# Performance work log

Hardware: AMD Instinct MI355X
Metric: run time of the kernel (lower is better)

The kernel has to match this reference:

```python
import jax, jax.numpy as jnp
import numpy as np

N_NODES = 10000
N_EDGES = 320000
D_NODE = 128
D_EDGE = 32
D_IN = 2 * D_NODE + D_EDGE  # 288, concat(sender, receiver, edge)
D_HID = 192                 # AutoMLP log-spaced hidden dim between 288 and 128
D_OUT = 128


def setup_inputs() -> dict:
    key = jax.random.key(0)
    ks = jax.random.split(key, 8)
    n_embed = jax.random.normal(ks[0], (N_NODES, D_NODE), dtype=jnp.float32)
    e_embed = jax.random.normal(ks[1], (N_EDGES, D_EDGE), dtype=jnp.float32)
    senders = jnp.sort(jax.random.randint(ks[2], (N_EDGES,), 0, N_NODES, dtype=jnp.int32))
    receivers = jax.random.randint(ks[3], (N_EDGES,), 0, N_NODES, dtype=jnp.int32)
    # AutoMLP parameters (lecun_normal-style scaling)
    W1 = jax.random.normal(ks[4], (D_IN, D_HID), dtype=jnp.float32) / np.sqrt(D_IN)
    b1 = jnp.zeros((D_HID,), dtype=jnp.float32)
    W2 = jax.random.normal(ks[5], (D_HID, D_OUT), dtype=jnp.float32) / np.sqrt(D_HID)
    b2 = jnp.zeros((D_OUT,), dtype=jnp.float32)
    return {"n_embed": n_embed, "e_embed": e_embed, "senders": senders,
            "receivers": receivers, "W1": W1, "b1": b1, "W2": W2, "b2": b2}


def reference(n_embed, e_embed, senders, receivers, W1, b1, W2, b2):
    # gather sender/receiver node embeddings and concat with edge features: [E, 288]
    inp = jnp.concatenate([n_embed[senders], n_embed[receivers], e_embed], axis=-1)
    # AutoMLP: Dense -> tanh -> Dense (final layer linear)
    h = jnp.tanh(inp @ W1 + b1)          # [E, 192]
    msg = h @ W2 + b2                    # [E, 128]
    # segment_mean over senders (sorted), num_segments = n_nodes
    seg_sum = jax.ops.segment_sum(msg, senders, num_segments=N_NODES,
                                  indices_are_sorted=True)
    counts = jax.ops.segment_sum(jnp.ones((msg.shape[0],), dtype=msg.dtype), senders,
                                 num_segments=N_NODES, indices_are_sorted=True)
    return seg_sum / jnp.maximum(counts, 1.0)[:, None]
```

## Files before the change

### kernel.cpp

```cpp
#include <hip/hip_runtime.h>

#define E_TOT 320000
#define NN    10000
#define DN    128
#define DE    32
#define DH    192
#define DO    128
#define EB    64
#define SHS   196

typedef __attribute__((ext_vector_type(8))) short bf16x8;
typedef __attribute__((ext_vector_type(4))) float f32x4;

#define W1_FRAGS (8*12*64)
#define E_FRAGS  (12*64)
#define W2_FRAGS (6*8*64)
#define FRAGS_TOT (W1_FRAGS + E_FRAGS + W2_FRAGS)
__device__ __align__(16) unsigned short g_p1[W1_FRAGS * 8];
__device__ __align__(16) unsigned short g_e [E_FRAGS * 8];
__device__ __align__(16) unsigned short g_p2[W2_FRAGS * 8];

__device__ __forceinline__ unsigned short f2bf(float f) {
    union { float f; unsigned u; } v; v.f = f;
    return (unsigned short)((v.u + 0x7FFFu + ((v.u >> 16) & 1u)) >> 16);
}
__device__ __forceinline__ float bflo(unsigned u) {
    union { unsigned v; float f; } t; t.v = u << 16; return t.f;
}
__device__ __forceinline__ float bfhi(unsigned u) {
    union { unsigned v; float f; } t; t.v = u & 0xFFFF0000u; return t.f;
}
__device__ __forceinline__ float bf2f(unsigned short s) {
    union { unsigned v; float f; } t; t.v = (unsigned)s << 16; return t.f;
}
__device__ __forceinline__ float tanh_fast(float x) {
    float ex = __expf(x + x);
    return 1.0f - 2.0f * __builtin_amdgcn_rcpf(ex + 1.0f);
}
__device__ __forceinline__ unsigned cvt_pk_bf16(float lo, float hi) {
    unsigned r;
    asm("v_cvt_pk_bf16_f32 %0, %1, %2" : "=v"(r) : "v"(lo), "v"(hi));
    return r;
}

__global__ void prep(const float* __restrict__ W1, const float* __restrict__ W2)
{
    int f = blockIdx.x * 256 + threadIdx.x;
    unsigned short tmp[8];
    if (f < W1_FRAGS) {
        int kk = f / (12 * 64), nt = (f >> 6) % 12, lane = f & 63;
        int r0 = kk * 32 + ((lane >> 4) << 3);
        int c  = nt * 16 + (lane & 15);
        #pragma unroll
        for (int i = 0; i < 8; ++i) tmp[i] = f2bf(W1[(r0 + i) * DH + c]);
        *(uint4*)(g_p1 + (size_t)f * 8) = *(const uint4*)tmp;
    } else if (f < W1_FRAGS + E_FRAGS) {
        int f2 = f - W1_FRAGS;
        int mt = f2 >> 6, lane = f2 & 63;
        int k0 = ((lane >> 4) << 3);
        int hid = mt * 16 + (lane & 15);
        #pragma unroll
        for (int i = 0; i < 8; ++i) tmp[i] = f2bf(W1[(256 + k0 + i) * DH + hid]);
        *(uint4*)(g_e + (size_t)f2 * 8) = *(const uint4*)tmp;
    } else if (f < FRAGS_TOT) {
        int f3 = f - W1_FRAGS - E_FRAGS;
        int kk = f3 / (8 * 64), nt = (f3 >> 6) % 8, lane = f3 & 63;
        int r0 = kk * 32 + ((lane >> 4) << 3);
        int c  = nt * 16 + (lane & 15);
        #pragma unroll
        for (int i = 0; i < 8; ++i) tmp[i] = f2bf(W2[(r0 + i) * DO + c]);
        *(uint4*)(g_p2 + (size_t)f3 * 8) = *(const uint4*)tmp;
    }
}

__global__ __launch_bounds__(256) void node_proj(
    const float* __restrict__ n_embed, const float* __restrict__ b1,
    unsigned short* __restrict__ P)
{
    __shared__ __align__(16) unsigned short s_a[64][136];
    const int tid  = threadIdx.x;
    const int half = blockIdx.y;
    const int n0   = blockIdx.x * 64;

    #pragma unroll
    for (int it = 0; it < 8; ++it) {
        int idx = tid + it * 256;
        int row = idx >> 5, c = idx & 31;
        float4 v = make_float4(0.f, 0.f, 0.f, 0.f);
        if (n0 + row < NN) v = ((const float4*)(n_embed + (size_t)(n0 + row) * DN))[c];
        unsigned t0 = cvt_pk_bf16(v.x, v.y), t1 = cvt_pk_bf16(v.z, v.w);
        *(uint2*)&s_a[row][c * 4] = make_uint2(t0, t1);
    }
    __syncthreads();

    const int lane = tid & 63, w = tid >> 6;
    const int arow = lane & 15, akb = (lane >> 4) * 8, rbase = (lane >> 4) * 4;

    f32x4 acc[4][3];
    #pragma unroll
    for (int mt = 0; mt < 4; ++mt)
        #pragma unroll
        for (int j = 0; j < 3; ++j) acc[mt][j] = (f32x4){0.f, 0.f, 0.f, 0.f};

    for (int kk = 0; kk < 4; ++kk) {
        bf16x8 a[4], b[3];
        #pragma unroll
        for (int mt = 0; mt < 4; ++mt)
            a[mt] = *(const bf16x8*)&s_a[mt * 16 + arow][kk * 32 + akb];
        #pragma unroll
        for (int j = 0; j < 3; ++j)
            b[j] = *(const bf16x8*)(g_p1 + (((size_t)(kk + 4 * half) * 12 + (3 * w + j)) * 64 + lane) * 8);
        #pragma unroll
        for (int mt = 0; mt < 4; ++mt)
            #pragma unroll
            for (int j = 0; j < 3; ++j)
                acc[mt][j] = __builtin_amdgcn_mfma_f32_16x16x32_bf16(a[mt], b[j], acc[mt][j], 0, 0, 0);
    }

    unsigned short* Pout = P + (size_t)half * NN * DH;
    float bj[3];
    #pragma unroll
    for (int j = 0; j < 3; ++j) bj[j] = (half == 0) ? b1[48 * w + 16 * j + arow] : 0.f;
    const int gq = arow >> 2, ii = arow & 3;
    #pragma unroll
    for (int mt = 0; mt < 4; ++mt)
        #pragma unroll
        for (int j = 0; j < 3; ++j)
            #pragma unroll
            for (int r = 0; r < 4; ++r) {
                int row = n0 + mt * 16 + rbase + r;
                if (row < NN)
                    Pout[((size_t)row * 4 + gq) * 48 + (3 * w + j) * 4 + ii] =
                        f2bf(acc[mt][j][r] + bj[j]);
            }
}

__global__ __launch_bounds__(256) void edge_reduce(
    const float* __restrict__ e_embed,
    const int* __restrict__ senders, const int* __restrict__ receivers,
    const unsigned short* __restrict__ Ps, const unsigned short* __restrict__ Pr,
    float* __restrict__ Hbar)
{
    __shared__ __align__(16) unsigned short s_h[EB][SHS];
    __shared__ int s_send[EB];

    const int tid  = threadIdx.x;
    const int nb8  = gridDim.x >> 3;
    const int e0   = (((blockIdx.x & 7) * nb8) + (blockIdx.x >> 3)) * EB;
    const int lane = tid & 63, w = tid >> 6;
    const int arow = lane & 15, g = lane >> 4;

    const int myedge = e0 + w * 16 + arow;
    const int sN = senders[myedge], rN = receivers[myedge];
    const unsigned short* psbase = Ps + ((size_t)sN * 4 + g) * 48;
    const unsigned short* prbase = Pr + ((size_t)rN * 4 + g) * 48;
    uint4 psq[6], prq[6];
    #pragma unroll
    for (int j = 0; j < 6; ++j) {
        psq[j] = *(const uint4*)(psbase + j * 8);
        prq[j] = *(const uint4*)(prbase + j * 8);
    }
    union { bf16x8 v; unsigned u[4]; } bfr;
    {
        const float* erow = e_embed + (size_t)myedge * DE + g * 8;
        float4 ev0 = *(const float4*)erow;
        float4 ev1 = *(const float4*)(erow + 4);
        bfr.u[0] = cvt_pk_bf16(ev0.x, ev0.y);
        bfr.u[1] = cvt_pk_bf16(ev0.z, ev0.w);
        bfr.u[2] = cvt_pk_bf16(ev1.x, ev1.y);
        bfr.u[3] = cvt_pk_bf16(ev1.z, ev1.w);
    }
    if (tid < EB) s_send[tid] = senders[e0 + tid];

    #pragma unroll
    for (int mt = 0; mt < 12; ++mt) {
        unsigned px, py, qx, qy;
        if ((mt & 1) == 0) {
            px = psq[mt >> 1].x; py = psq[mt >> 1].y;
            qx = prq[mt >> 1].x; qy = prq[mt >> 1].y;
        } else {
            px = psq[mt >> 1].z; py = psq[mt >> 1].w;
            qx = prq[mt >> 1].z; qy = prq[mt >> 1].w;
        }
        bf16x8 af = *(const bf16x8*)(g_e + ((size_t)mt * 64 + lane) * 8);
        f32x4 z = (f32x4){0.f, 0.f, 0.f, 0.f};
        f32x4 acc = __builtin_amdgcn_mfma_f32_16x16x32_bf16(af, bfr.v, z, 0, 0, 0);
        float t0 = tanh_fast(acc[0] + bflo(px) + bflo(qx));
        float t1 = tanh_fast(acc[1] + bfhi(px) + bfhi(qx));
        float t2 = tanh_fast(acc[2] + bflo(py) + bflo(qy));
        float t3 = tanh_fast(acc[3] + bfhi(py) + bfhi(qy));
        *(uint2*)&s_h[w * 16 + arow][mt * 16 + g * 4] =
            make_uint2(cvt_pk_bf16(t0, t1), cvt_pk_bf16(t2, t3));
    }
    __syncthreads();

    if (tid < DH) {
        const int c = tid;
        float sum = 0.f;
        int cur = s_send[0];
        #pragma unroll 8
        for (int e = 0; e < EB; ++e) {
            sum += bf2f(s_h[e][c]);
            int nxt = (e + 1 < EB) ? s_send[e + 1] : -1;
            if (nxt != cur) {
                atomicAdd(&Hbar[(size_t)cur * DH + c], sum);
                sum = 0.f;
                cur = nxt;
            }
        }
    }
}

__global__ __launch_bounds__(256) void node_out(
    const float* __restrict__ Hbar, const int* __restrict__ senders,
    const float* __restrict__ b2, float* __restrict__ out)
{
    const int tid  = threadIdx.x;
    const int lane = tid & 63, w = tid >> 6;
    const int n0   = (blockIdx.x * 4 + w) * 16;
    if (n0 >= NN) return;
    const int arow = lane & 15, akb = (lane >> 4) * 8, rbase = (lane >> 4) * 4;

    const int myrow = (n0 + arow < NN) ? (n0 + arow) : (NN - 1);
    float ic;
    {
        int lo = 0, hi = E_TOT;
        while (lo < hi) { int m = (lo + hi) >> 1; if (senders[m] < myrow) lo = m + 1; else hi = m; }
        int s0 = lo;
        hi = E_TOT;
        while (lo < hi) { int m = (lo + hi) >> 1; if (senders[m] < myrow + 1) lo = m + 1; else hi = m; }
        int cnt = lo - s0;
        ic = (cnt > 0) ? 1.0f / (float)cnt : 0.0f;
    }

    const float* hrow = Hbar + (size_t)myrow * DH;
    union { bf16x8 v; unsigned u[4]; } a[6];
    #pragma unroll
    for (int kk = 0; kk < 6; ++kk) {
        float4 v0 = *(const float4*)(hrow + kk * 32 + akb);
        float4 v1 = *(const float4*)(hrow + kk * 32 + akb + 4);
        a[kk].u[0] = cvt_pk_bf16(v0.x * ic, v0.y * ic);
        a[kk].u[1] = cvt_pk_bf16(v0.z * ic, v0.w * ic);
        a[kk].u[2] = cvt_pk_bf16(v1.x * ic, v1.y * ic);
        a[kk].u[3] = cvt_pk_bf16(v1.z * ic, v1.w * ic);
    }

    f32x4 acc[8];
    #pragma unroll
    for (int j = 0; j < 8; ++j) acc[j] = (f32x4){0.f, 0.f, 0.f, 0.f};

    #pragma unroll
    for (int kk = 0; kk < 6; ++kk)
        #pragma unroll
        for (int j = 0; j < 8; ++j) {
            bf16x8 b = *(const bf16x8*)(g_p2 + (((size_t)kk * 8 + j) * 64 + lane) * 8);
            acc[j] = __builtin_amdgcn_mfma_f32_16x16x32_bf16(a[kk].v, b, acc[j], 0, 0, 0);
        }

    #pragma unroll
    for (int j = 0; j < 8; ++j) {
        const float bd = b2[j * 16 + arow];
        #pragma unroll
        for (int r = 0; r < 4; ++r) {
            int row = n0 + rbase + r;
            if (row < NN)
                out[(size_t)row * DO + j * 16 + arow] = acc[j][r] + bd;
        }
    }
}

extern "C" void kernel_launch(void* const* d_in, const int* in_sizes, int n_in,
                              void* d_out, int out_size, void* d_ws, size_t ws_size,
                              hipStream_t stream)
{
    const float* n_embed   = (const float*)d_in[0];
    const float* e_embed   = (const float*)d_in[1];
    const int*   senders   = (const int*)d_in[2];
    const int*   receivers = (const int*)d_in[3];
    const float* W1        = (const float*)d_in[4];
    const float* b1        = (const float*)d_in[5];
    const float* W2        = (const float*)d_in[6];
    const float* b2        = (const float*)d_in[7];
    float* out = (float*)d_out;

    unsigned short* Ps = (unsigned short*)d_ws;
    unsigned short* Pr = Ps + (size_t)NN * DH;
    float*          Hbar = (float*)(Pr + (size_t)NN * DH);

    hipMemsetAsync(Hbar, 0, (size_t)NN * DH * sizeof(float), stream);
    prep<<<(FRAGS_TOT + 255) / 256, 256, 0, stream>>>(W1, W2);
    node_proj<<<dim3((NN + 63) / 64, 2), 256, 0, stream>>>(n_embed, b1, Ps);
    edge_reduce<<<E_TOT / EB, 256, 0, stream>>>(
        e_embed, senders, receivers, Ps, Pr, Hbar);
    node_out<<<(NN + 63) / 64, 256, 0, stream>>>(Hbar, senders, b2, out);
}
```

Baseline: 92.26 us.

## Fold memset and CSR row_start into prep, feed bias via MFMA accumulator

The Hbar zeroing memset moves into the prep kernel, and prep also builds a CSR row_start array from the sorted senders. node_out then reads segment counts from row_start instead of doing two binary searches per row. In edge_reduce the per-edge projected sender and receiver terms are passed as the MFMA accumulator initial value rather than added after the MFMA. The aim is to remove one launch, the divergent binary-search loads and a few VALU adds, in exchange for a larger prep grid and extra workspace.

Result: faster. 79.23 us (-14.1%).

```diff
diff --git a/kernel.cpp b/kernel.cpp
--- a/kernel.cpp
+++ b/kernel.cpp
@@ -16,6 +16,7 @@
 #define E_FRAGS  (12*64)
 #define W2_FRAGS (6*8*64)
 #define FRAGS_TOT (W1_FRAGS + E_FRAGS + W2_FRAGS)
+#define ZH (NN * DH / 4)
 __device__ __align__(16) unsigned short g_p1[W1_FRAGS * 8];
 __device__ __align__(16) unsigned short g_e [E_FRAGS * 8];
 __device__ __align__(16) unsigned short g_p2[W2_FRAGS * 8];
@@ -43,7 +44,9 @@
     return r;
 }
 
-__global__ void prep(const float* __restrict__ W1, const float* __restrict__ W2)
+__global__ void prep(const float* __restrict__ W1, const float* __restrict__ W2,
+                     const int* __restrict__ senders,
+                     float* __restrict__ Hbar, int* __restrict__ row_start)
 {
     int f = blockIdx.x * 256 + threadIdx.x;
     unsigned short tmp[8];
@@ -70,6 +73,16 @@
         #pragma unroll
         for (int i = 0; i < 8; ++i) tmp[i] = f2bf(W2[(r0 + i) * DO + c]);
         *(uint4*)(g_p2 + (size_t)f3 * 8) = *(const uint4*)tmp;
+    } else if (f < FRAGS_TOT + ZH) {
+        ((float4*)Hbar)[f - FRAGS_TOT] = make_float4(0.f, 0.f, 0.f, 0.f);
+    } else if (f < FRAGS_TOT + ZH + E_TOT) {
+        int e = f - FRAGS_TOT - ZH;
+        int s_cur  = senders[e];
+        int s_prev = (e == 0) ? -1 : senders[e - 1];
+        if (s_prev != s_cur)
+            for (int n = s_prev + 1; n <= s_cur; ++n) row_start[n] = e;
+        if (e == E_TOT - 1)
+            for (int n = s_cur + 1; n <= NN; ++n) row_start[n] = E_TOT;
     }
 }
 
@@ -182,13 +195,17 @@
             px = psq[mt >> 1].z; py = psq[mt >> 1].w;
             qx = prq[mt >> 1].z; qy = prq[mt >> 1].w;
         }
+        f32x4 cinit;
+        cinit[0] = bflo(px) + bflo(qx);
+        cinit[1] = bfhi(px) + bfhi(qx);
+        cinit[2] = bflo(py) + bflo(qy);
+        cinit[3] = bfhi(py) + bfhi(qy);
         bf16x8 af = *(const bf16x8*)(g_e + ((size_t)mt * 64 + lane) * 8);
-        f32x4 z = (f32x4){0.f, 0.f, 0.f, 0.f};
-        f32x4 acc = __builtin_amdgcn_mfma_f32_16x16x32_bf16(af, bfr.v, z, 0, 0, 0);
-        float t0 = tanh_fast(acc[0] + bflo(px) + bflo(qx));
-        float t1 = tanh_fast(acc[1] + bfhi(px) + bfhi(qx));
-        float t2 = tanh_fast(acc[2] + bflo(py) + bflo(qy));
-        float t3 = tanh_fast(acc[3] + bfhi(py) + bfhi(qy));
+        f32x4 acc = __builtin_amdgcn_mfma_f32_16x16x32_bf16(af, bfr.v, cinit, 0, 0, 0);
+        float t0 = tanh_fast(acc[0]);
+        float t1 = tanh_fast(acc[1]);
+        float t2 = tanh_fast(acc[2]);
+        float t3 = tanh_fast(acc[3]);
         *(uint2*)&s_h[w * 16 + arow][mt * 16 + g * 4] =
             make_uint2(cvt_pk_bf16(t0, t1), cvt_pk_bf16(t2, t3));
     }
@@ -212,7 +229,7 @@
 }
 
 __global__ __launch_bounds__(256) void node_out(
-    const float* __restrict__ Hbar, const int* __restrict__ senders,
+    const float* __restrict__ Hbar, const int* __restrict__ row_start,
     const float* __restrict__ b2, float* __restrict__ out)
 {
     const int tid  = threadIdx.x;
@@ -222,16 +239,8 @@
     const int arow = lane & 15, akb = (lane >> 4) * 8, rbase = (lane >> 4) * 4;
 
     const int myrow = (n0 + arow < NN) ? (n0 + arow) : (NN - 1);
-    float ic;
-    {
-        int lo = 0, hi = E_TOT;
-        while (lo < hi) { int m = (lo + hi) >> 1; if (senders[m] < myrow) lo = m + 1; else hi = m; }
-        int s0 = lo;
-        hi = E_TOT;
-        while (lo < hi) { int m = (lo + hi) >> 1; if (senders[m] < myrow + 1) lo = m + 1; else hi = m; }
-        int cnt = lo - s0;
-        ic = (cnt > 0) ? 1.0f / (float)cnt : 0.0f;
-    }
+    const int cnt = row_start[myrow + 1] - row_start[myrow];
+    const float ic = (cnt > 0) ? 1.0f / (float)cnt : 0.0f;
 
     const float* hrow = Hbar + (size_t)myrow * DH;
     union { bf16x8 v; unsigned u[4]; } a[6];
@@ -283,14 +292,15 @@
     const float* b2        = (const float*)d_in[7];
     float* out = (float*)d_out;
 
-    unsigned short* Ps = (unsigned short*)d_ws;
-    unsigned short* Pr = Ps + (size_t)NN * DH;
+    unsigned short* Ps   = (unsigned short*)d_ws;
+    unsigned short* Pr   = Ps + (size_t)NN * DH;
     float*          Hbar = (float*)(Pr + (size_t)NN * DH);
-
-    hipMemsetAsync(Hbar, 0, (size_t)NN * DH * sizeof(float), stream);
-    prep<<<(FRAGS_TOT + 255) / 256, 256, 0, stream>>>(W1, W2);
+    int*            row_start = (int*)(Hbar + (size_t)NN * DH);
+
+    const int prep_items = FRAGS_TOT + ZH + E_TOT;
+    prep<<<(prep_items + 255) / 256, 256, 0, stream>>>(W1, W2, senders, Hbar, row_start);
     node_proj<<<dim3((NN + 63) / 64, 2), 256, 0, stream>>>(n_embed, b1, Ps);
     edge_reduce<<<E_TOT / EB, 256, 0, stream>>>(
         e_embed, senders, receivers, Ps, Pr, Hbar);
-    node_out<<<(NN + 63) / 64, 256, 0, stream>>>(Hbar, senders, b2, out);
-}
+    node_out<<<(NN + 63) / 64, 256, 0, stream>>>(Hbar, row_start, b2, out);
+}
```
